# Optimization experiments

Measured on AMD Instinct MI355X. Metric: run time of the kernel, lower is better.

## Reference

```python
import jax, jax.numpy as jnp
import numpy as np

N_EMBD = 384
N_HEADS = 6
HEAD_SIZE = N_EMBD // N_HEADS  # 64
LN_EPS = 1e-5


def _layernorm(x, g, b):
    mu = jnp.mean(x, axis=-1, keepdims=True)
    var = jnp.var(x, axis=-1, keepdims=True)
    return (x - mu) * jax.lax.rsqrt(var + LN_EPS) * g + b


def setup_inputs() -> dict:
    key = jax.random.key(0)
    ks = jax.random.split(key, 12)
    B, T, C, H, D = 128, 256, N_EMBD, N_HEADS, HEAD_SIZE
    s_in = 1.0 / np.sqrt(C)
    s_ff = 1.0 / np.sqrt(4 * C)
    return {
        "x": jax.random.normal(ks[0], (B, T, C), dtype=jnp.float32),
        "ln1_g": jnp.ones((C,), jnp.float32),
        "ln1_b": jnp.zeros((C,), jnp.float32),
        "Wq": jax.random.uniform(ks[1], (H, C, D), jnp.float32, -s_in, s_in),
        "Wk": jax.random.uniform(ks[2], (H, C, D), jnp.float32, -s_in, s_in),
        "Wv": jax.random.uniform(ks[3], (H, C, D), jnp.float32, -s_in, s_in),
        "Wo": jax.random.uniform(ks[4], (C, C), jnp.float32, -s_in, s_in),
        "bo": jnp.zeros((C,), jnp.float32),
        "ln2_g": jnp.ones((C,), jnp.float32),
        "ln2_b": jnp.zeros((C,), jnp.float32),
        "W1": jax.random.uniform(ks[5], (C, 4 * C), jnp.float32, -s_in, s_in),
        "b1": jnp.zeros((4 * C,), jnp.float32),
        "W2": jax.random.uniform(ks[6], (4 * C, C), jnp.float32, -s_ff, s_ff),
        "b2": jnp.zeros((C,), jnp.float32),
    }


def reference(x, ln1_g, ln1_b, Wq, Wk, Wv, Wo, bo, ln2_g, ln2_b, W1, b1, W2, b2):
    # Dropout layers are identity (eval mode).
    B, T, C = x.shape
    h = _layernorm(x, ln1_g, ln1_b)
    # Per-head projections: [B,T,C] x [H,C,D] -> [B,H,T,D]
    q = jnp.einsum('btc,hcd->bhtd', h, Wq)
    k = jnp.einsum('btc,hcd->bhtd', h, Wk)
    v = jnp.einsum('btc,hcd->bhtd', h, Wv)
    scale = HEAD_SIZE ** (-0.5)
    scores = jnp.einsum('bhtd,bhsd->bhts', q, k) * scale  # [B,H,T,T]
    causal = jnp.tril(jnp.ones((T, T), dtype=bool))
    scores = jnp.where(causal, scores, jnp.float32(-jnp.inf))
    wei = jax.nn.softmax(scores, axis=-1)
    attn = jnp.einsum('bhts,bhsd->bhtd', wei, v)  # [B,H,T,D]
    attn = attn.transpose(0, 2, 1, 3).reshape(B, T, C)  # concat heads
    x = x + attn @ Wo + bo
    h2 = _layernorm(x, ln2_g, ln2_b)
    ff = jax.nn.relu(h2 @ W1 + b1) @ W2 + b2
    return x + ff
```

## Files before the change

### kernel.cpp

```cpp
#include <hip/hip_runtime.h>

typedef unsigned int u32;
typedef unsigned short u16;
typedef __bf16 bf16_t;
typedef float f32x4 __attribute__((ext_vector_type(4)));
typedef bf16_t bfrag __attribute__((ext_vector_type(8)));
typedef u16 u16x8 __attribute__((ext_vector_type(8)));

__device__ inline u16 f2bf(float f) {
    union { float f; u32 u; } v; v.f = f;
    u32 r = v.u + 0x7fffu + ((v.u >> 16) & 1u);
    return (u16)(r >> 16);
}
__device__ inline float bf2f(u16 h) {
    union { u32 u; float f; } v; v.u = ((u32)h) << 16; return v.f;
}

__device__ inline f32x4 mfma16(bfrag a, bfrag b, f32x4 c) {
    return __builtin_amdgcn_mfma_f32_16x16x32_bf16(a, b, c, 0, 0, 0);
}

__device__ inline void gload_lds16(const void* g, void* l) {
    __builtin_amdgcn_global_load_lds((const __attribute__((address_space(1))) u32*)g,
                                     (__attribute__((address_space(3))) u32*)l, 16, 0, 0);
}

__device__ inline float redmax16(float v) {
    #pragma unroll
    for (int m = 1; m < 16; m <<= 1) v = fmaxf(v, __shfl_xor(v, m));
    return v;
}
__device__ inline float redsum16(float v) {
    #pragma unroll
    for (int m = 1; m < 16; m <<= 1) v += __shfl_xor(v, m);
    return v;
}

#define NTOK 32768
#define QKV_ELEMS 12582912

__global__ __launch_bounds__(256) void prep_weights(
    const float* __restrict__ Wq, const float* __restrict__ Wk,
    const float* __restrict__ Wv, const float* __restrict__ Wo,
    const float* __restrict__ W1, const float* __restrict__ W2,
    u16* __restrict__ wqkvT, u16* __restrict__ woT,
    u16* __restrict__ w1T, u16* __restrict__ w2T)
{
    __shared__ float tile[64][65];
    const int b = blockIdx.x;
    const float* src; u16* dst;
    int sr0, sc0, srs, dr0, dc0, drs;
    if (b < 36) {
        int i = b / 6, j = b - i * 6;
        src = Wo;  srs = 384;  sr0 = i * 64; sc0 = j * 64;
        dst = woT; drs = 384;  dr0 = j * 64; dc0 = i * 64;
    } else if (b < 180) {
        int t = b - 36; int i = t / 24, j = t - i * 24;
        src = W1;  srs = 1536; sr0 = i * 64; sc0 = j * 64;
        dst = w1T; drs = 384;  dr0 = j * 64; dc0 = i * 64;
    } else if (b < 324) {
        int t = b - 180; int i = t / 6, j = t - i * 6;
        src = W2;  srs = 384;  sr0 = i * 64; sc0 = j * 64;
        dst = w2T; drs = 1536; dr0 = j * 64; dc0 = i * 64;
    } else {
        int t = b - 324;
        int m2 = t / 36; t -= m2 * 36;
        int h = t / 6, tt = t - h * 6;
        src = (m2 == 0) ? Wq : ((m2 == 1) ? Wk : Wv);
        srs = 64;  sr0 = h * 384 + tt * 64; sc0 = 0;
        dst = wqkvT; drs = 384; dr0 = m2 * 384 + h * 64; dc0 = tt * 64;
    }
    const int lane = threadIdx.x & 63, grp = threadIdx.x >> 6;
    #pragma unroll
    for (int i = 0; i < 16; i++) {
        int r = grp * 16 + i;
        tile[r][lane] = src[(size_t)(sr0 + r) * srs + sc0 + lane];
    }
    __syncthreads();
    #pragma unroll
    for (int i = 0; i < 16; i++) {
        int r = grp * 16 + i;
        dst[(size_t)(dr0 + r) * drs + dc0 + lane] = f2bf(tile[lane][r]);
    }
}

__global__ __launch_bounds__(256) void ln_f32(
    const float* __restrict__ x, const float* __restrict__ g,
    const float* __restrict__ b, u16* __restrict__ out)
{
    const int row = blockIdx.x * 4 + (threadIdx.x >> 6);
    const int lane = threadIdx.x & 63;
    const float2* xr = (const float2*)(x + (size_t)row * 384);
    float2 v[3];
    float s = 0.f, s2 = 0.f;
    #pragma unroll
    for (int i = 0; i < 3; i++) {
        v[i] = xr[lane + i * 64];
        s += v[i].x + v[i].y; s2 += v[i].x * v[i].x + v[i].y * v[i].y;
    }
    #pragma unroll
    for (int m = 1; m < 64; m <<= 1) { s += __shfl_xor(s, m); s2 += __shfl_xor(s2, m); }
    float mean = s * (1.f / 384.f);
    float rstd = rsqrtf(s2 * (1.f / 384.f) - mean * mean + 1e-5f);
    u32* op = (u32*)(out + (size_t)row * 384);
    #pragma unroll
    for (int i = 0; i < 3; i++) {
        int c = (lane + i * 64) * 2;
        u32 lo = f2bf((v[i].x - mean) * rstd * g[c] + b[c]);
        u32 hi = f2bf((v[i].y - mean) * rstd * g[c + 1] + b[c + 1]);
        op[lane + i * 64] = lo | (hi << 16);
    }
}

__global__ __launch_bounds__(256) void ln_bf16(
    const u16* __restrict__ x, const float* __restrict__ g,
    const float* __restrict__ b, u16* __restrict__ out)
{
    const int row = blockIdx.x * 4 + (threadIdx.x >> 6);
    const int lane = threadIdx.x & 63;
    const u32* xr = (const u32*)(x + (size_t)row * 384);
    float vx[3], vy[3];
    float s = 0.f, s2 = 0.f;
    #pragma unroll
    for (int i = 0; i < 3; i++) {
        u32 w = xr[lane + i * 64];
        vx[i] = bf2f((u16)(w & 0xffffu));
        vy[i] = bf2f((u16)(w >> 16));
        s += vx[i] + vy[i]; s2 += vx[i] * vx[i] + vy[i] * vy[i];
    }
    #pragma unroll
    for (int m = 1; m < 64; m <<= 1) { s += __shfl_xor(s, m); s2 += __shfl_xor(s2, m); }
    float mean = s * (1.f / 384.f);
    float rstd = rsqrtf(s2 * (1.f / 384.f) - mean * mean + 1e-5f);
    u32* op = (u32*)(out + (size_t)row * 384);
    #pragma unroll
    for (int i = 0; i < 3; i++) {
        int c = (lane + i * 64) * 2;
        u32 lo = f2bf((vx[i] - mean) * rstd * g[c] + b[c]);
        u32 hi = f2bf((vy[i] - mean) * rstd * g[c + 1] + b[c + 1]);
        op[lane + i * 64] = lo | (hi << 16);
    }
}

template<int EPI, int NT>
__global__ __launch_bounds__(256, 4) void gemm_m97(
    const u16* __restrict__ A, const u16* __restrict__ Bt,
    const float* __restrict__ bias, const void* __restrict__ resid,
    void* __restrict__ outp, int M, int N)
{
    const int K = NT * 64;
    __shared__ __align__(16) u16 As[128 * 64];
    __shared__ __align__(16) u16 Bs[128 * 64];
    const int tid = threadIdx.x, wave = tid >> 6, lane = tid & 63;
    const int nbn = N >> 7;
    const int nwg = gridDim.x;
    const int bid = blockIdx.x;
    const int wg = (bid & 7) * (nwg >> 3) + (bid >> 3);
    const int bm = wg / nbn, bn = wg - bm * nbn;
    const int rowA0 = bm << 7, rowB0 = bn << 7;
    const int wm = (wave >> 1) << 6, wn = (wave & 1) << 6;
    const int lr = lane >> 3, lc = lane & 7;
    f32x4 acc[4][4] = {};

    for (int t = 0; t < NT; ++t) {
        const int ko = t << 6;
        #pragma unroll
        for (int p = 0; p < 4; p++) {
            const int idx = p * 4 + wave;
            const int r = idx * 8 + lr;
            const int csrc = ((lc ^ (r & 7)) << 3);
            gload_lds16(A + (size_t)(rowA0 + r) * K + ko + csrc, &As[idx * 512]);
            gload_lds16(Bt + (size_t)(rowB0 + r) * K + ko + csrc, &Bs[idx * 512]);
        }
        __syncthreads();
        #pragma unroll
        for (int kk = 0; kk < 2; kk++) {
            bfrag af[4], bfr[4];
            #pragma unroll
            for (int mt = 0; mt < 4; mt++) {
                const int row = wm + mt * 16 + (lane & 15);
                af[mt] = *(const bfrag*)((const char*)As + row * 128 +
                          (((kk * 4 + (lane >> 4)) ^ (row & 7)) << 4));
            }
            #pragma unroll
            for (int nt = 0; nt < 4; nt++) {
                const int row = wn + nt * 16 + (lane & 15);
                bfr[nt] = *(const bfrag*)((const char*)Bs + row * 128 +
                          (((kk * 4 + (lane >> 4)) ^ (row & 7)) << 4));
            }
            #pragma unroll
            for (int mt = 0; mt < 4; mt++)
                #pragma unroll
                for (int nt = 0; nt < 4; nt++)
                    acc[mt][nt] = mfma16(af[mt], bfr[nt], acc[mt][nt]);
        }
        __syncthreads();
    }

    #pragma unroll
    for (int mt = 0; mt < 4; mt++) {
        #pragma unroll
        for (int nt = 0; nt < 4; nt++) {
            #pragma unroll
            for (int r2 = 0; r2 < 4; r2++) {
                const int gr = rowA0 + wm + mt * 16 + ((lane >> 4) << 2) + r2;
                const int gc = rowB0 + wn + nt * 16 + (lane & 15);
                float v = acc[mt][nt][r2];
                if constexpr (EPI == 0) {
                    int m2 = gc / 384;
                    int rem = gc - m2 * 384;
                    int hh = rem >> 6, d = rem & 63;
                    if (m2 == 0) v *= 0.125f;
                    int bb = gr >> 8, t2 = gr & 255;
                    ((u16*)outp)[(size_t)m2 * QKV_ELEMS +
                                 ((size_t)((bb * 6 + hh) * 256 + t2) << 6) + d] = f2bf(v);
                } else if constexpr (EPI == 1) {
                    ((u16*)outp)[(size_t)gr * N + gc] =
                        f2bf(((const float*)resid)[(size_t)gr * N + gc] + bias[gc] + v);
                } else if constexpr (EPI == 2) {
                    float t2 = v + bias[gc];
                    ((u16*)outp)[(size_t)gr * N + gc] = f2bf(t2 > 0.f ? t2 : 0.f);
                } else {
                    ((float*)outp)[(size_t)gr * N + gc] =
                        bf2f(((const u16*)resid)[(size_t)gr * N + gc]) + bias[gc] + v;
                }
            }
        }
    }
}

__global__ __launch_bounds__(512) void attn_kernel(
    const u16* __restrict__ q, const u16* __restrict__ k, const u16* __restrict__ v,
    u16* __restrict__ outp)
{
    __shared__ __align__(16) u16 Ks[256 * 64];
    __shared__ __align__(16) u16 Vt[64 * 256];
    __shared__ __align__(16) u16 Ps[8 * 512];
    const int bh = blockIdx.x;
    const int tid = threadIdx.x, wave = tid >> 6, lane = tid & 63;
    const u16* qb = q + (size_t)bh * 16384;
    const u16* kb = k + (size_t)bh * 16384;
    const u16* vb = v + (size_t)bh * 16384;

    #pragma unroll
    for (int p = 0; p < 4; p++) {
        const int idx = p * 8 + wave;
        const int r = idx * 8 + (lane >> 3);
        const int csrc = (((lane & 7) ^ (r & 7)) << 3);
        gload_lds16(kb + (size_t)r * 64 + csrc, &Ks[idx * 512]);
    }
    #pragma unroll
    for (int p = 0; p < 4; p++) {
        const int e = (p * 512 + tid) * 8;
        const int key = e >> 6, d0 = e & 63;
        u16x8 raw = *(const u16x8*)(vb + (size_t)key * 64 + d0);
        #pragma unroll
        for (int j = 0; j < 8; j++) {
            const int d = d0 + j;
            Vt[d * 256 + (((key >> 3) ^ (d & 7)) << 3) + (key & 7)] = raw[j];
        }
    }
    __syncthreads();

    const int bI = bh / 6, hh = bh - bI * 6;

    #pragma unroll
    for (int t = 0; t < 2; t++) {
        const int qtile = (t == 0) ? wave : (15 - wave);
        const int qrowbase = qtile * 16;
        bfrag qf[2];
        {
            const int r = qrowbase + (lane & 15);
            qf[0] = *(const bfrag*)(qb + (size_t)r * 64 + ((lane >> 4) << 3));
            qf[1] = *(const bfrag*)(qb + (size_t)r * 64 + 32 + ((lane >> 4) << 3));
        }
        f32x4 S[16];
        #pragma unroll
        for (int kt = 0; kt < 16; kt++) {
            if (kt <= qtile) {
                f32x4 s = {0.f, 0.f, 0.f, 0.f};
                const int key = kt * 16 + (lane & 15);
                const char* kbase = (const char*)Ks + key * 128;
                s = mfma16(qf[0], *(const bfrag*)(kbase + ((((lane >> 4)) ^ (key & 7)) << 4)), s);
                s = mfma16(qf[1], *(const bfrag*)(kbase + (((4 + (lane >> 4)) ^ (key & 7)) << 4)), s);
                if (kt == qtile) {
                    const int qit = (lane >> 4) << 2;
                    #pragma unroll
                    for (int r2 = 0; r2 < 4; r2++)
                        if ((lane & 15) > qit + r2) s[r2] = -1e30f;
                }
                S[kt] = s;
            }
        }
        float mx[4] = {-1e30f, -1e30f, -1e30f, -1e30f};
        #pragma unroll
        for (int kt = 0; kt < 16; kt++) if (kt <= qtile)
            #pragma unroll
            for (int r2 = 0; r2 < 4; r2++) mx[r2] = fmaxf(mx[r2], S[kt][r2]);
        #pragma unroll
        for (int r2 = 0; r2 < 4; r2++) mx[r2] = redmax16(mx[r2]);
        float sm[4] = {0.f, 0.f, 0.f, 0.f};
        #pragma unroll
        for (int kt = 0; kt < 16; kt++) if (kt <= qtile)
            #pragma unroll
            for (int r2 = 0; r2 < 4; r2++) {
                float p = __expf(S[kt][r2] - mx[r2]);
                S[kt][r2] = p; sm[r2] += p;
            }
        #pragma unroll
        for (int r2 = 0; r2 < 4; r2++) sm[r2] = redsum16(sm[r2]);

        f32x4 O[4] = {};
        u16* Pw = &Ps[wave * 512];
        const int nch = (qtile + 2) >> 1;
        #pragma unroll
        for (int ch = 0; ch < 8; ch++) {
            if (ch < nch) {
                #pragma unroll
                for (int ktl = 0; ktl < 2; ktl++) {
                    const int kt = ch * 2 + ktl;
                    const int keyl = ktl * 16 + (lane & 15);
                    const int cidx = keyl >> 3;
                    #pragma unroll
                    for (int r2 = 0; r2 < 4; r2++) {
                        const int qq = ((lane >> 4) << 2) + r2;
                        float pv = (kt <= qtile) ? S[kt][r2] : 0.f;
                        Pw[qq * 32 + ((cidx ^ (qq & 3)) << 3) + (keyl & 7)] = f2bf(pv);
                    }
                }
                const int qq = lane & 15;
                bfrag pa = *(const bfrag*)(Pw + qq * 32 + (((lane >> 4) ^ (qq & 3)) << 3));
                #pragma unroll
                for (int dt = 0; dt < 4; dt++) {
                    const int d = dt * 16 + (lane & 15);
                    const int cc = ch * 4 + (lane >> 4);
                    bfrag vf = *(const bfrag*)((const char*)Vt + d * 512 + ((cc ^ (d & 7)) << 4));
                    O[dt] = mfma16(pa, vf, O[dt]);
                }
            }
        }
        #pragma unroll
        for (int dt = 0; dt < 4; dt++) {
            #pragma unroll
            for (int r2 = 0; r2 < 4; r2++) {
                const int qg = qrowbase + ((lane >> 4) << 2) + r2;
                const float val = O[dt][r2] / sm[r2];
                outp[(size_t)(bI * 256 + qg) * 384 + hh * 64 + dt * 16 + (lane & 15)] = f2bf(val);
            }
        }
    }
}

extern "C" void kernel_launch(void* const* d_in, const int* in_sizes, int n_in,
                              void* d_out, int out_size, void* d_ws, size_t ws_size,
                              hipStream_t stream)
{
    const float* x    = (const float*)d_in[0];
    const float* ln1g = (const float*)d_in[1];
    const float* ln1b = (const float*)d_in[2];
    const float* Wq   = (const float*)d_in[3];
    const float* Wk   = (const float*)d_in[4];
    const float* Wv   = (const float*)d_in[5];
    const float* Wo   = (const float*)d_in[6];
    const float* bo   = (const float*)d_in[7];
    const float* ln2g = (const float*)d_in[8];
    const float* ln2b = (const float*)d_in[9];
    const float* W1   = (const float*)d_in[10];
    const float* b1   = (const float*)d_in[11];
    const float* W2   = (const float*)d_in[12];
    const float* b2   = (const float*)d_in[13];

    if (ws_size < 230031360u) return;

    char* ws = (char*)d_ws;
    u16*   wqkvT = (u16*)(ws + 0);
    u16*   woT   = (u16*)(ws + 884736);
    u16*   w1T   = (u16*)(ws + 1179648);
    u16*   w2T   = (u16*)(ws + 2359296);
    u16*   hbuf  = (u16*)(ws + 3538944);
    u16*   qbuf  = (u16*)(ws + 28704768);
    u16*   kbuf  = (u16*)(ws + 53870592);
    u16*   vbuf  = (u16*)(ws + 79036416);
    u16*   x2h   = (u16*)(ws + 104202240);
    u16*   mid   = (u16*)(ws + 129368064);
    float* out   = (float*)d_out;

    prep_weights<<<432, 256, 0, stream>>>(Wq, Wk, Wv, Wo, W1, W2, wqkvT, woT, w1T, w2T);
    ln_f32<<<8192, 256, 0, stream>>>(x, ln1g, ln1b, hbuf);
    gemm_m97<0, 6><<<2304, 256, 0, stream>>>(hbuf, wqkvT, nullptr, nullptr, qbuf,
                                             NTOK, 1152);
    attn_kernel<<<768, 512, 0, stream>>>(qbuf, kbuf, vbuf, hbuf);
    gemm_m97<1, 6><<<768, 256, 0, stream>>>(hbuf, woT, bo, x, x2h, NTOK, 384);
    ln_bf16<<<8192, 256, 0, stream>>>(x2h, ln2g, ln2b, qbuf);
    gemm_m97<2, 6><<<3072, 256, 0, stream>>>(qbuf, w1T, b1, nullptr, mid, NTOK, 1536);
    gemm_m97<3, 24><<<768, 256, 0, stream>>>(mid, w2T, b2, x2h, out, NTOK, 384);
}
```

Measured before the change: 230.2 us.

## Use persistent B-stationary GEMM for K=384 projections with triple-buffered A stream

Adds a persistent GEMM kernel where each workgroup loads its full 128-column B panel (K=384) into LDS once, then loops over many 128-row A tiles with a 3-slot async global-to-LDS pipeline. The kernel replaces the QKV, output-projection and FFN-up GEMMs, launching about one workgroup per CU. The goal is to cut repeated weight loads and launch/tail overhead. In exchange it uses 144KB of LDS and one workgroup per CU, so it relies on the pipeline to hide latency rather than on occupancy.

```diff
diff --git a/kernel.cpp b/kernel.cpp
--- a/kernel.cpp
+++ b/kernel.cpp
@@ -142,6 +142,127 @@
     }
 }
 
+template<int EPI, int NBN>
+__global__ __launch_bounds__(512, 1) void gemm_pb(
+    const u16* __restrict__ A, const u16* __restrict__ Bt,
+    const float* __restrict__ bias, const void* __restrict__ resid,
+    void* __restrict__ outp, int G_CNT)
+{
+    const int K = 384, NKC = 6, N = NBN * 128;
+    __shared__ __align__(16) u16 smem[73728];
+    u16* Bs = smem;
+    u16* Ar = smem + 49152;
+    const int tid = threadIdx.x, wave = tid >> 6, lane = tid & 63;
+    const int lr = lane >> 3, lc = lane & 7;
+    const int nwg = gridDim.x, bid = blockIdx.x;
+    const int qx = nwg >> 3, rx = nwg & 7, xc = bid & 7, ii = bid >> 3;
+    const int wg = (xc < rx ? xc * (qx + 1) : rx * (qx + 1) + (xc - rx) * qx) + ii;
+    const int g = wg / NBN, bn = wg - g * NBN;
+    const int rowB0 = bn << 7;
+    const int wm = (wave >> 1) << 5, wn = (wave & 1) << 6;
+
+    #pragma unroll
+    for (int s = 0; s < NKC; s++)
+        #pragma unroll
+        for (int p = 0; p < 2; p++) {
+            const int idx = p * 8 + wave;
+            const int r = idx * 8 + lr;
+            gload_lds16(Bt + (size_t)(rowB0 + r) * K + s * 64 + ((lc ^ (r & 7)) << 3),
+                        &Bs[s * 8192 + idx * 512]);
+        }
+    asm volatile("s_waitcnt vmcnt(0)" ::: "memory");
+    __syncthreads();
+
+    const int ntiles = (256 - g + G_CNT - 1) / G_CNT;
+    const int U = ntiles * NKC;
+    f32x4 acc[2][4] = {};
+
+#define STAGE_A(u)                                                                   \
+    {                                                                                \
+        const int t_ = (u) / NKC, s_ = (u) - t_ * NKC, sl_ = (u) % 3;                \
+        const int rA0_ = (g + t_ * G_CNT) << 7;                                      \
+        _Pragma("unroll")                                                            \
+        for (int p = 0; p < 2; p++) {                                                \
+            const int idx = p * 8 + wave;                                            \
+            const int r = idx * 8 + lr;                                              \
+            gload_lds16(A + (size_t)(rA0_ + r) * K + s_ * 64 + ((lc ^ (r & 7)) << 3),\
+                        &Ar[sl_ * 8192 + idx * 512]);                                \
+        }                                                                            \
+    }
+
+    STAGE_A(0);
+    if (U > 1) STAGE_A(1);
+
+    for (int u = 0; u < U; ++u) {
+        if (u + 2 < U) {
+            STAGE_A(u + 2);
+            asm volatile("s_waitcnt vmcnt(4)" ::: "memory");
+        } else if (u + 1 < U) {
+            asm volatile("s_waitcnt vmcnt(2)" ::: "memory");
+        } else {
+            asm volatile("s_waitcnt vmcnt(0)" ::: "memory");
+        }
+        __builtin_amdgcn_s_barrier();
+        const int s = u % NKC;
+        const char* Ab = (const char*)&Ar[(u % 3) * 8192];
+        const char* Bb = (const char*)&Bs[s * 8192];
+        #pragma unroll
+        for (int kk = 0; kk < 2; kk++) {
+            bfrag af[2], bfr[4];
+            #pragma unroll
+            for (int mt = 0; mt < 2; mt++) {
+                const int row = wm + mt * 16 + (lane & 15);
+                af[mt] = *(const bfrag*)(Ab + row * 128 +
+                          (((kk * 4 + (lane >> 4)) ^ (row & 7)) << 4));
+            }
+            #pragma unroll
+            for (int nt = 0; nt < 4; nt++) {
+                const int row = wn + nt * 16 + (lane & 15);
+                bfr[nt] = *(const bfrag*)(Bb + row * 128 +
+                          (((kk * 4 + (lane >> 4)) ^ (row & 7)) << 4));
+            }
+            #pragma unroll
+            for (int mt = 0; mt < 2; mt++)
+                #pragma unroll
+                for (int nt = 0; nt < 4; nt++)
+                    acc[mt][nt] = mfma16(af[mt], bfr[nt], acc[mt][nt]);
+        }
+        if (s == NKC - 1) {
+            const int rowA0 = (g + (u / NKC) * G_CNT) << 7;
+            #pragma unroll
+            for (int mt = 0; mt < 2; mt++) {
+                #pragma unroll
+                for (int nt = 0; nt < 4; nt++) {
+                    #pragma unroll
+                    for (int r2 = 0; r2 < 4; r2++) {
+                        const int gr = rowA0 + wm + mt * 16 + ((lane >> 4) << 2) + r2;
+                        const int gc = rowB0 + wn + nt * 16 + (lane & 15);
+                        float v = acc[mt][nt][r2];
+                        if constexpr (EPI == 0) {
+                            int m2 = gc / 384;
+                            int rem = gc - m2 * 384;
+                            int hh = rem >> 6, d = rem & 63;
+                            if (m2 == 0) v *= 0.125f;
+                            int bb = gr >> 8, t2 = gr & 255;
+                            ((u16*)outp)[(size_t)m2 * QKV_ELEMS +
+                                         ((size_t)((bb * 6 + hh) * 256 + t2) << 6) + d] = f2bf(v);
+                        } else if constexpr (EPI == 1) {
+                            ((u16*)outp)[(size_t)gr * N + gc] =
+                                f2bf(((const float*)resid)[(size_t)gr * N + gc] + bias[gc] + v);
+                        } else {
+                            float t2 = v + bias[gc];
+                            ((u16*)outp)[(size_t)gr * N + gc] = f2bf(t2 > 0.f ? t2 : 0.f);
+                        }
+                    }
+                    acc[mt][nt] = (f32x4){0.f, 0.f, 0.f, 0.f};
+                }
+            }
+        }
+        __builtin_amdgcn_s_barrier();
+    }
+#undef STAGE_A
+}
+
 template<int EPI, int NT>
 __global__ __launch_bounds__(256, 4) void gemm_m97(
     const u16* __restrict__ A, const u16* __restrict__ Bt,
@@ -206,24 +327,8 @@
                 const int gr = rowA0 + wm + mt * 16 + ((lane >> 4) << 2) + r2;
                 const int gc = rowB0 + wn + nt * 16 + (lane & 15);
                 float v = acc[mt][nt][r2];
-                if constexpr (EPI == 0) {
-                    int m2 = gc / 384;
-                    int rem = gc - m2 * 384;
-                    int hh = rem >> 6, d = rem & 63;
-                    if (m2 == 0) v *= 0.125f;
-                    int bb = gr >> 8, t2 = gr & 255;
-                    ((u16*)outp)[(size_t)m2 * QKV_ELEMS +
-                                 ((size_t)((bb * 6 + hh) * 256 + t2) << 6) + d] = f2bf(v);
-                } else if constexpr (EPI == 1) {
-                    ((u16*)outp)[(size_t)gr * N + gc] =
-                        f2bf(((const float*)resid)[(size_t)gr * N + gc] + bias[gc] + v);
-                } else if constexpr (EPI == 2) {
-                    float t2 = v + bias[gc];
-                    ((u16*)outp)[(size_t)gr * N + gc] = f2bf(t2 > 0.f ? t2 : 0.f);
-                } else {
-                    ((float*)outp)[(size_t)gr * N + gc] =
-                        bf2f(((const u16*)resid)[(size_t)gr * N + gc]) + bias[gc] + v;
-                }
+                ((float*)outp)[(size_t)gr * N + gc] =
+                    bf2f(((const u16*)resid)[(size_t)gr * N + gc]) + bias[gc] + v;
             }
         }
     }
@@ -387,11 +492,10 @@
 
     prep_weights<<<432, 256, 0, stream>>>(Wq, Wk, Wv, Wo, W1, W2, wqkvT, woT, w1T, w2T);
     ln_f32<<<8192, 256, 0, stream>>>(x, ln1g, ln1b, hbuf);
-    gemm_m97<0, 6><<<2304, 256, 0, stream>>>(hbuf, wqkvT, nullptr, nullptr, qbuf,
-                                             NTOK, 1152);
+    gemm_pb<0, 9><<<252, 512, 0, stream>>>(hbuf, wqkvT, nullptr, nullptr, qbuf, 28);
     attn_kernel<<<768, 512, 0, stream>>>(qbuf, kbuf, vbuf, hbuf);
-    gemm_m97<1, 6><<<768, 256, 0, stream>>>(hbuf, woT, bo, x, x2h, NTOK, 384);
+    gemm_pb<1, 3><<<255, 512, 0, stream>>>(hbuf, woT, bo, x, x2h, 85);
     ln_bf16<<<8192, 256, 0, stream>>>(x2h, ln2g, ln2b, qbuf);
-    gemm_m97<2, 6><<<3072, 256, 0, stream>>>(qbuf, w1T, b1, nullptr, mid, NTOK, 1536);
+    gemm_pb<2, 12><<<252, 512, 0, stream>>>(qbuf, w1T, b1, nullptr, mid, 21);
     gemm_m97<3, 24><<<768, 256, 0, stream>>>(mid, w2T, b2, x2h, out, NTOK, 384);
 }
```

Result: slower. 260.6 us (+13.2%).

## Rewrite GEMM as 8-wave 256x128 tile with triple-buffered prefetch; move residual into LN2

Applied to the files above, without the earlier changes.

Replaces the 4-wave 128x128 GEMM with an 8-wave kernel that computes a 256x128 tile. It triple-buffers LDS stages, issuing global-to-LDS loads two K-steps ahead in the gaps between MFMA groups, and raises wave priority (setprio) during the MFMAs. The out-projection GEMM now writes only the raw product, and a new LN kernel adds the residual and bias, writes x2 and the normalized h2 in one pass. This is meant to hide memory latency behind compute and cut launch overhead, at the cost of more LDS (144KB per block), more barriers, and an extra bf16 round-trip through the kbuf scratch buffer.

```diff
diff --git a/kernel.cpp b/kernel.cpp
--- a/kernel.cpp
+++ b/kernel.cpp
@@ -6,6 +6,8 @@
 typedef float f32x4 __attribute__((ext_vector_type(4)));
 typedef bf16_t bfrag __attribute__((ext_vector_type(8)));
 typedef u16 u16x8 __attribute__((ext_vector_type(8)));
+
+#define WAIT_VMCNT(n) asm volatile("s_waitcnt vmcnt(" #n ")" ::: "memory")
 
 __device__ inline u16 f2bf(float f) {
     union { float f; u32 u; } v; v.f = f;
@@ -112,90 +114,163 @@
     }
 }
 
-__global__ __launch_bounds__(256) void ln_bf16(
-    const u16* __restrict__ x, const float* __restrict__ g,
-    const float* __restrict__ b, u16* __restrict__ out)
+__global__ __launch_bounds__(256) void ln_resid(
+    const float* __restrict__ x, const u16* __restrict__ wout,
+    const float* __restrict__ bo, const float* __restrict__ g,
+    const float* __restrict__ b, u16* __restrict__ x2h, u16* __restrict__ h2)
 {
     const int row = blockIdx.x * 4 + (threadIdx.x >> 6);
     const int lane = threadIdx.x & 63;
-    const u32* xr = (const u32*)(x + (size_t)row * 384);
-    float vx[3], vy[3];
+    const float2* xr = (const float2*)(x + (size_t)row * 384);
+    const u32* wr = (const u32*)(wout + (size_t)row * 384);
+    float tx[3], ty[3];
     float s = 0.f, s2 = 0.f;
     #pragma unroll
     for (int i = 0; i < 3; i++) {
-        u32 w = xr[lane + i * 64];
-        vx[i] = bf2f((u16)(w & 0xffffu));
-        vy[i] = bf2f((u16)(w >> 16));
-        s += vx[i] + vy[i]; s2 += vx[i] * vx[i] + vy[i] * vy[i];
+        float2 xv = xr[lane + i * 64];
+        u32 w = wr[lane + i * 64];
+        int c = (lane + i * 64) * 2;
+        tx[i] = xv.x + bf2f((u16)(w & 0xffffu)) + bo[c];
+        ty[i] = xv.y + bf2f((u16)(w >> 16)) + bo[c + 1];
+        s += tx[i] + ty[i]; s2 += tx[i] * tx[i] + ty[i] * ty[i];
     }
     #pragma unroll
     for (int m = 1; m < 64; m <<= 1) { s += __shfl_xor(s, m); s2 += __shfl_xor(s2, m); }
     float mean = s * (1.f / 384.f);
     float rstd = rsqrtf(s2 * (1.f / 384.f) - mean * mean + 1e-5f);
-    u32* op = (u32*)(out + (size_t)row * 384);
+    u32* xo = (u32*)(x2h + (size_t)row * 384);
+    u32* ho = (u32*)(h2 + (size_t)row * 384);
     #pragma unroll
     for (int i = 0; i < 3; i++) {
         int c = (lane + i * 64) * 2;
-        u32 lo = f2bf((vx[i] - mean) * rstd * g[c] + b[c]);
-        u32 hi = f2bf((vy[i] - mean) * rstd * g[c + 1] + b[c + 1]);
-        op[lane + i * 64] = lo | (hi << 16);
+        xo[lane + i * 64] = (u32)f2bf(tx[i]) | ((u32)f2bf(ty[i]) << 16);
+        u32 lo = f2bf((tx[i] - mean) * rstd * g[c] + b[c]);
+        u32 hi = f2bf((ty[i] - mean) * rstd * g[c + 1] + b[c + 1]);
+        ho[lane + i * 64] = lo | (hi << 16);
     }
 }
 
 template<int EPI, int NT>
-__global__ __launch_bounds__(256, 4) void gemm_m97(
+__global__ __launch_bounds__(512, 2) void gemm_8p(
     const u16* __restrict__ A, const u16* __restrict__ Bt,
     const float* __restrict__ bias, const void* __restrict__ resid,
     void* __restrict__ outp, int M, int N)
 {
     const int K = NT * 64;
-    __shared__ __align__(16) u16 As[128 * 64];
-    __shared__ __align__(16) u16 Bs[128 * 64];
+    __shared__ __align__(16) u16 smem[73728];
     const int tid = threadIdx.x, wave = tid >> 6, lane = tid & 63;
     const int nbn = N >> 7;
-    const int nwg = gridDim.x;
-    const int bid = blockIdx.x;
+    const int nwg = gridDim.x, bid = blockIdx.x;
     const int wg = (bid & 7) * (nwg >> 3) + (bid >> 3);
     const int bm = wg / nbn, bn = wg - bm * nbn;
-    const int rowA0 = bm << 7, rowB0 = bn << 7;
+    const int rowA0 = bm << 8, rowB0 = bn << 7;
     const int wm = (wave >> 1) << 6, wn = (wave & 1) << 6;
     const int lr = lane >> 3, lc = lane & 7;
     f32x4 acc[4][4] = {};
 
+#define STAGE_A(u, i)                                                               \
+    {                                                                               \
+        const int c_ = (i) * 8 + wave;                                              \
+        const int r_ = c_ * 8 + lr;                                                 \
+        gload_lds16(A + (size_t)(rowA0 + r_) * K + ((u) << 6) + ((lc ^ (r_ & 7)) << 3), \
+                    &smem[((u) % 3) * 24576 + c_ * 512]);                           \
+    }
+#define STAGE_B(u, i)                                                               \
+    {                                                                               \
+        const int c_ = (i) * 8 + wave;                                              \
+        const int r_ = c_ * 8 + lr;                                                 \
+        gload_lds16(Bt + (size_t)(rowB0 + r_) * K + ((u) << 6) + ((lc ^ (r_ & 7)) << 3), \
+                    &smem[((u) % 3) * 24576 + 16384 + c_ * 512]);                   \
+    }
+
+    STAGE_A(0, 0) STAGE_A(0, 1) STAGE_A(0, 2) STAGE_A(0, 3) STAGE_B(0, 0) STAGE_B(0, 1)
+    if (NT > 1) {
+        STAGE_A(1, 0) STAGE_A(1, 1) STAGE_A(1, 2) STAGE_A(1, 3) STAGE_B(1, 0) STAGE_B(1, 1)
+    }
+
     for (int t = 0; t < NT; ++t) {
-        const int ko = t << 6;
-        #pragma unroll
-        for (int p = 0; p < 4; p++) {
-            const int idx = p * 4 + wave;
-            const int r = idx * 8 + lr;
-            const int csrc = ((lc ^ (r & 7)) << 3);
-            gload_lds16(A + (size_t)(rowA0 + r) * K + ko + csrc, &As[idx * 512]);
-            gload_lds16(Bt + (size_t)(rowB0 + r) * K + ko + csrc, &Bs[idx * 512]);
-        }
-        __syncthreads();
-        #pragma unroll
-        for (int kk = 0; kk < 2; kk++) {
-            bfrag af[4], bfr[4];
-            #pragma unroll
-            for (int mt = 0; mt < 4; mt++) {
-                const int row = wm + mt * 16 + (lane & 15);
-                af[mt] = *(const bfrag*)((const char*)As + row * 128 +
-                          (((kk * 4 + (lane >> 4)) ^ (row & 7)) << 4));
-            }
-            #pragma unroll
-            for (int nt = 0; nt < 4; nt++) {
-                const int row = wn + nt * 16 + (lane & 15);
-                bfr[nt] = *(const bfrag*)((const char*)Bs + row * 128 +
-                          (((kk * 4 + (lane >> 4)) ^ (row & 7)) << 4));
-            }
-            #pragma unroll
-            for (int mt = 0; mt < 4; mt++)
-                #pragma unroll
-                for (int nt = 0; nt < 4; nt++)
-                    acc[mt][nt] = mfma16(af[mt], bfr[nt], acc[mt][nt]);
-        }
-        __syncthreads();
-    }
+        if (t + 1 < NT) { WAIT_VMCNT(6); } else { WAIT_VMCNT(0); }
+        __builtin_amdgcn_s_barrier();
+        const char* Ab = (const char*)&smem[(t % 3) * 24576];
+        const char* Bb = Ab + 32768;
+        const bool pf = (t + 2 < NT);
+        bfrag af[4], bf01[2], bf23[2];
+
+        #pragma unroll
+        for (int mt = 0; mt < 4; mt++) {
+            const int row = wm + mt * 16 + (lane & 15);
+            af[mt] = *(const bfrag*)(Ab + row * 128 + ((((lane >> 4)) ^ (row & 7)) << 4));
+        }
+        #pragma unroll
+        for (int nt = 0; nt < 2; nt++) {
+            const int row = wn + nt * 16 + (lane & 15);
+            bf01[nt] = *(const bfrag*)(Bb + row * 128 + ((((lane >> 4)) ^ (row & 7)) << 4));
+        }
+        if (pf) { STAGE_A(t + 2, 0) STAGE_A(t + 2, 1) }
+        __builtin_amdgcn_s_barrier();
+        __builtin_amdgcn_s_setprio(1);
+        #pragma unroll
+        for (int mt = 0; mt < 4; mt++)
+            #pragma unroll
+            for (int nt = 0; nt < 2; nt++)
+                acc[mt][nt] = mfma16(af[mt], bf01[nt], acc[mt][nt]);
+        __builtin_amdgcn_s_setprio(0);
+        __builtin_amdgcn_s_barrier();
+
+        #pragma unroll
+        for (int nt = 0; nt < 2; nt++) {
+            const int row = wn + (nt + 2) * 16 + (lane & 15);
+            bf23[nt] = *(const bfrag*)(Bb + row * 128 + ((((lane >> 4)) ^ (row & 7)) << 4));
+        }
+        if (pf) { STAGE_A(t + 2, 2) STAGE_A(t + 2, 3) }
+        __builtin_amdgcn_s_barrier();
+        __builtin_amdgcn_s_setprio(1);
+        #pragma unroll
+        for (int mt = 0; mt < 4; mt++)
+            #pragma unroll
+            for (int nt = 0; nt < 2; nt++)
+                acc[mt][nt + 2] = mfma16(af[mt], bf23[nt], acc[mt][nt + 2]);
+        __builtin_amdgcn_s_setprio(0);
+        __builtin_amdgcn_s_barrier();
+
+        #pragma unroll
+        for (int mt = 0; mt < 4; mt++) {
+            const int row = wm + mt * 16 + (lane & 15);
+            af[mt] = *(const bfrag*)(Ab + row * 128 + (((4 + (lane >> 4)) ^ (row & 7)) << 4));
+        }
+        #pragma unroll
+        for (int nt = 0; nt < 2; nt++) {
+            const int row = wn + nt * 16 + (lane & 15);
+            bf01[nt] = *(const bfrag*)(Bb + row * 128 + (((4 + (lane >> 4)) ^ (row & 7)) << 4));
+        }
+        if (pf) { STAGE_B(t + 2, 0) STAGE_B(t + 2, 1) }
+        __builtin_amdgcn_s_barrier();
+        __builtin_amdgcn_s_setprio(1);
+        #pragma unroll
+        for (int mt = 0; mt < 4; mt++)
+            #pragma unroll
+            for (int nt = 0; nt < 2; nt++)
+                acc[mt][nt] = mfma16(af[mt], bf01[nt], acc[mt][nt]);
+        __builtin_amdgcn_s_setprio(0);
+        __builtin_amdgcn_s_barrier();
+
+        #pragma unroll
+        for (int nt = 0; nt < 2; nt++) {
+            const int row = wn + (nt + 2) * 16 + (lane & 15);
+            bf23[nt] = *(const bfrag*)(Bb + row * 128 + (((4 + (lane >> 4)) ^ (row & 7)) << 4));
+        }
+        __builtin_amdgcn_s_barrier();
+        __builtin_amdgcn_s_setprio(1);
+        #pragma unroll
+        for (int mt = 0; mt < 4; mt++)
+            #pragma unroll
+            for (int nt = 0; nt < 2; nt++)
+                acc[mt][nt + 2] = mfma16(af[mt], bf23[nt], acc[mt][nt + 2]);
+        __builtin_amdgcn_s_setprio(0);
+        __builtin_amdgcn_s_barrier();
+    }
+#undef STAGE_A
+#undef STAGE_B
 
     #pragma unroll
     for (int mt = 0; mt < 4; mt++) {
@@ -215,8 +290,7 @@
                     ((u16*)outp)[(size_t)m2 * QKV_ELEMS +
                                  ((size_t)((bb * 6 + hh) * 256 + t2) << 6) + d] = f2bf(v);
                 } else if constexpr (EPI == 1) {
-                    ((u16*)outp)[(size_t)gr * N + gc] =
-                        f2bf(((const float*)resid)[(size_t)gr * N + gc] + bias[gc] + v);
+                    ((u16*)outp)[(size_t)gr * N + gc] = f2bf(v);
                 } else if constexpr (EPI == 2) {
                     float t2 = v + bias[gc];
                     ((u16*)outp)[(size_t)gr * N + gc] = f2bf(t2 > 0.f ? t2 : 0.f);
@@ -387,11 +461,11 @@
 
     prep_weights<<<432, 256, 0, stream>>>(Wq, Wk, Wv, Wo, W1, W2, wqkvT, woT, w1T, w2T);
     ln_f32<<<8192, 256, 0, stream>>>(x, ln1g, ln1b, hbuf);
-    gemm_m97<0, 6><<<2304, 256, 0, stream>>>(hbuf, wqkvT, nullptr, nullptr, qbuf,
-                                             NTOK, 1152);
+    gemm_8p<0, 6><<<1152, 512, 0, stream>>>(hbuf, wqkvT, nullptr, nullptr, qbuf,
+                                            NTOK, 1152);
     attn_kernel<<<768, 512, 0, stream>>>(qbuf, kbuf, vbuf, hbuf);
-    gemm_m97<1, 6><<<768, 256, 0, stream>>>(hbuf, woT, bo, x, x2h, NTOK, 384);
-    ln_bf16<<<8192, 256, 0, stream>>>(x2h, ln2g, ln2b, qbuf);
-    gemm_m97<2, 6><<<3072, 256, 0, stream>>>(qbuf, w1T, b1, nullptr, mid, NTOK, 1536);
-    gemm_m97<3, 24><<<768, 256, 0, stream>>>(mid, w2T, b2, x2h, out, NTOK, 384);
-}
+    gemm_8p<1, 6><<<384, 512, 0, stream>>>(hbuf, woT, nullptr, nullptr, kbuf, NTOK, 384);
+    ln_resid<<<8192, 256, 0, stream>>>(x, kbuf, bo, ln2g, ln2b, x2h, qbuf);
+    gemm_8p<2, 6><<<1536, 512, 0, stream>>>(qbuf, w1T, b1, nullptr, mid, NTOK, 1536);
+    gemm_8p<3, 24><<<384, 512, 0, stream>>>(mid, w2T, b2, x2h, out, NTOK, 384);
+}
```

New measurement: 258.4 us. 12.2% more time.
